# Performance work log

Measured on AMD Instinct MI355X. Metric: run time of the kernel, lower is better.

## Reference

```python
import jax, jax.numpy as jnp
import numpy as np
from math import sqrt

B, L, S = 4, 2048, 2048
D_MODEL, H = 1024, 16
E = D_MODEL // H  # head dim = 64


def setup_inputs() -> dict:
    key = jax.random.key(0)
    ks = jax.random.split(key, 11)
    s = 1.0 / sqrt(D_MODEL)
    return {
        "queries": jax.random.normal(ks[0], (B, L, D_MODEL), jnp.float32),
        "keys": jax.random.normal(ks[1], (B, S, D_MODEL), jnp.float32),
        "values": jax.random.normal(ks[2], (B, S, D_MODEL), jnp.float32),
        "Wq": jax.random.normal(ks[3], (D_MODEL, D_MODEL), jnp.float32) * s,
        "bq": jax.random.normal(ks[4], (D_MODEL,), jnp.float32) * s,
        "Wk": jax.random.normal(ks[5], (D_MODEL, D_MODEL), jnp.float32) * s,
        "bk": jax.random.normal(ks[6], (D_MODEL,), jnp.float32) * s,
        "Wv": jax.random.normal(ks[7], (D_MODEL, D_MODEL), jnp.float32) * s,
        "bv": jax.random.normal(ks[8], (D_MODEL,), jnp.float32) * s,
        "Wo": jax.random.normal(ks[9], (D_MODEL, D_MODEL), jnp.float32) * s,
        "bo": jax.random.normal(ks[10], (D_MODEL,), jnp.float32) * s,
    }


def reference(queries, keys, values, Wq, bq, Wk, bk, Wv, bv, Wo, bo):
    # QKV projections, split heads: [B, L/S, H, E]
    q = (queries @ Wq + bq).reshape(B, L, H, E)
    k = (keys @ Wk + bk).reshape(B, S, H, E)
    v = (values @ Wv + bv).reshape(B, S, H, E)
    scale = 1.0 / sqrt(E)
    scores = jnp.einsum('blhe,bshe->bhls', q, k)  # [B,H,L,S]
    A = jax.nn.softmax(scale * scores, axis=-1)   # dropout is identity in eval
    out = jnp.einsum('bhls,bshd->blhd', A, v).reshape(B, L, H * E)
    return out @ Wo + bo
```

## Files before the change

### kernel.cpp

```cpp
#include <hip/hip_runtime.h>
#include <hip/hip_bf16.h>

typedef unsigned short u16;
typedef unsigned int u32;
using short8 = __attribute__((ext_vector_type(8))) short;
using f32x4  = __attribute__((ext_vector_type(4))) float;
using f32x16 = __attribute__((ext_vector_type(16))) float;
using u32x2  = __attribute__((ext_vector_type(2))) unsigned int;
using u32x4  = __attribute__((ext_vector_type(4))) unsigned int;

#define B_  4
#define L_  2048
#define S_  2048
#define DM  1024
#define H_  16
#define E_  64

__device__ __forceinline__ u16 f2bf(float f) {
  union { float f; unsigned u; } v; v.f = f;
  unsigned u = v.u;
  unsigned r = (u + 0x7fffu + ((u >> 16) & 1u)) >> 16;
  return (u16)r;
}

__device__ __forceinline__ float exp2a(float x) {
  float r; asm("v_exp_f32 %0, %1" : "=v"(r) : "v"(x)); return r;
}

__device__ __forceinline__ u32 cvtpk(float lo, float hi) {
  u32 r; asm("v_cvt_pk_bf16_f32 %0, %1, %2" : "=v"(r) : "v"(lo), "v"(hi));
  return r;
}

__device__ __forceinline__ f32x4 mfma16(short8 a, short8 b, f32x4 c) {
  return __builtin_amdgcn_mfma_f32_16x16x32_bf16(a, b, c, 0, 0, 0);
}

__device__ __forceinline__ f32x16 mfma32(short8 a, short8 b, f32x16 c) {
  return __builtin_amdgcn_mfma_f32_32x32x16_bf16(a, b, c, 0, 0, 0);
}

__device__ __forceinline__ void gload_lds16(const u16* g, u16* l) {
  __builtin_amdgcn_global_load_lds(
      (const __attribute__((address_space(1))) unsigned int*)(const void*)g,
      (__attribute__((address_space(3))) unsigned int*)(void*)l, 16, 0, 0);
}

__global__ __launch_bounds__(256) void transp_all(const float* __restrict__ w0,
                                                  const float* __restrict__ w1,
                                                  const float* __restrict__ w2,
                                                  const float* __restrict__ w3,
                                                  u16* __restrict__ t0,
                                                  u16* __restrict__ t1,
                                                  u16* __restrict__ t2,
                                                  u16* __restrict__ t3) {
  const float* W = blockIdx.z == 0 ? w0 : blockIdx.z == 1 ? w1 :
                   blockIdx.z == 2 ? w2 : w3;
  u16* Wt = blockIdx.z == 0 ? t0 : blockIdx.z == 1 ? t1 :
            blockIdx.z == 2 ? t2 : t3;
  __shared__ float t[32][33];
  int tx = threadIdx.x & 31, ty = (threadIdx.x >> 5) & 7;
#pragma unroll
  for (int j = 0; j < 32; j += 8)
    t[ty + j][tx] = W[(size_t)(blockIdx.y * 32 + ty + j) * DM + blockIdx.x * 32 + tx];
  __syncthreads();
#pragma unroll
  for (int j = 0; j < 32; j += 8)
    Wt[(size_t)(blockIdx.x * 32 + ty + j) * DM + blockIdx.y * 32 + tx] = f2bf(t[tx][ty + j]);
}

template <int EPI>
__device__ __forceinline__ void gemm_body(const float* __restrict__ A,
                                          const u16* __restrict__ Bt,
                                          const float* __restrict__ bias,
                                          void* __restrict__ Cout,
                                          int M, int N, int K, float oscale,
                                          int bx, int by) {
  __shared__ u16 lA[128 * 32];
  __shared__ u16 lB[128 * 32];
  const int tid = threadIdx.x, wid = tid >> 6, lane = tid & 63;
  const int lr = lane & 15, lh = lane >> 4;
  const int m0 = by * 128, n0 = bx * 128;
  const int wr = wid >> 1, wc = wid & 1;

  f32x4 acc[4][4];
#pragma unroll
  for (int m = 0; m < 4; m++)
#pragma unroll
    for (int n = 0; n < 4; n++) acc[m][n] = (f32x4){0.f, 0.f, 0.f, 0.f};

  const int srow = wid * 16 + (lane >> 2);
  const int scol = (lane & 3) * 8;

  const float* a0p = A + (size_t)(m0 + srow) * K + scol;
  const float* a1p = A + (size_t)(m0 + 64 + srow) * K + scol;

  f32x4 r00 = *(const f32x4*)a0p;
  f32x4 r01 = *(const f32x4*)(a0p + 4);
  f32x4 r10 = *(const f32x4*)a1p;
  f32x4 r11 = *(const f32x4*)(a1p + 4);

  for (int k0 = 0; k0 < K; k0 += 32) {
    gload_lds16(Bt + (size_t)(n0 + srow) * K + k0 + scol, lB + (wid * 16) * 32);
    gload_lds16(Bt + (size_t)(n0 + 64 + srow) * K + k0 + scol, lB + (64 + wid * 16) * 32);
    u32x4 w0 = {cvtpk(r00.x, r00.y), cvtpk(r00.z, r00.w),
                cvtpk(r01.x, r01.y), cvtpk(r01.z, r01.w)};
    u32x4 w1 = {cvtpk(r10.x, r10.y), cvtpk(r10.z, r10.w),
                cvtpk(r11.x, r11.y), cvtpk(r11.z, r11.w)};
    *(u32x4*)(lA + (size_t)srow * 32 + scol) = w0;
    *(u32x4*)(lA + (size_t)(64 + srow) * 32 + scol) = w1;
    if (k0 + 32 < K) {
      r00 = *(const f32x4*)(a0p + k0 + 32);
      r01 = *(const f32x4*)(a0p + k0 + 36);
      r10 = *(const f32x4*)(a1p + k0 + 32);
      r11 = *(const f32x4*)(a1p + k0 + 36);
    }
    __syncthreads();
    short8 af[4], bf[4];
#pragma unroll
    for (int m = 0; m < 4; m++)
      af[m] = *(const short8*)(lA + (wr * 64 + m * 16 + lr) * 32 + lh * 8);
#pragma unroll
    for (int n = 0; n < 4; n++)
      bf[n] = *(const short8*)(lB + (wc * 64 + n * 16 + lr) * 32 + lh * 8);
#pragma unroll
    for (int m = 0; m < 4; m++)
#pragma unroll
      for (int n = 0; n < 4; n++) acc[m][n] = mfma16(af[m], bf[n], acc[m][n]);
    __syncthreads();
  }

#pragma unroll
  for (int m = 0; m < 4; m++) {
    int grow0 = m0 + wr * 64 + m * 16 + lh * 4;
#pragma unroll
    for (int n = 0; n < 4; n++) {
      int gcol = n0 + wc * 64 + n * 16 + lr;
      float bi = bias[gcol];
      float v0 = (acc[m][n][0] + bi) * oscale;
      float v1 = (acc[m][n][1] + bi) * oscale;
      float v2 = (acc[m][n][2] + bi) * oscale;
      float v3 = (acc[m][n][3] + bi) * oscale;
      u32 p01 = cvtpk(v0, v1), p23 = cvtpk(v2, v3);
      u16* C = (u16*)Cout;
#pragma unroll
      for (int r = 0; r < 4; r++) {
        u32 pk = r < 2 ? p01 : p23;
        u16 bv = (r & 1) ? (u16)(pk >> 16) : (u16)(pk & 0xffff);
        int grow = grow0 + r;
        if constexpr (EPI == 0) {
          C[(size_t)grow * N + gcol] = bv;
        } else {
          int bb = grow >> 11, sl = grow & 2047;
          C[((size_t)(bb * DM) + gcol) * S_ + sl] = bv;
        }
      }
    }
  }
}

__global__ __launch_bounds__(256) void gemm_qkv(
    const float* __restrict__ q, const float* __restrict__ k, const float* __restrict__ v,
    const u16* __restrict__ WqT, const u16* __restrict__ WkT, const u16* __restrict__ WvT,
    const float* __restrict__ bq, const float* __restrict__ bk, const float* __restrict__ bv,
    u16* __restrict__ Qp, u16* __restrict__ Kp, u16* __restrict__ Vt, float qsc) {
  int lin = blockIdx.x;
  int swz = (lin & 7) * 192 + (lin >> 3);
  const int bx = swz & 7, by = (swz >> 3) & 63, z = swz >> 9;
  if (z == 0)
    gemm_body<0>(q, WqT, bq, Qp, B_ * L_, DM, DM, qsc, bx, by);
  else if (z == 1)
    gemm_body<0>(k, WkT, bk, Kp, B_ * L_, DM, DM, 1.0f, bx, by);
  else
    gemm_body<1>(v, WvT, bv, Vt, B_ * L_, DM, DM, 1.0f, bx, by);
}

__global__ __launch_bounds__(256) void gemm_out(const u16* __restrict__ A,
                                                const u16* __restrict__ Bt,
                                                const float* __restrict__ bias,
                                                float* __restrict__ C) {
  const int N = DM, K = DM;
  int lin = blockIdx.x;
  int swz = (lin & 7) * 64 + (lin >> 3);
  const int bx = swz & 7, by = swz >> 3;

  __shared__ u16 lA[128 * 128];
  __shared__ u16 lB[128 * 128];
  const int tid = threadIdx.x, wid = tid >> 6, lane = tid & 63;
  const int lr = lane & 15, lh = lane >> 4;
  const int m0 = by * 128, n0 = bx * 128;
  const int wr = wid >> 1, wc = wid & 1;

  f32x4 acc[4][4];
#pragma unroll
  for (int m = 0; m < 4; m++)
#pragma unroll
    for (int n = 0; n < 4; n++) acc[m][n] = (f32x4){0.f, 0.f, 0.f, 0.f};

  const int srw = wid * 4 + (lane >> 4);
  const int scx = ((lane & 15) ^ (srw & 15)) * 8;
  const u16* As = A + (size_t)(m0 + srw) * K + scx;
  const u16* Bs = Bt + (size_t)(n0 + srw) * K + scx;
  u16* lAw = lA + (wid * 4) * 128;
  u16* lBw = lB + (wid * 4) * 128;

  for (int k0 = 0; k0 < K; k0 += 128) {
#pragma unroll
    for (int p = 0; p < 8; p++) {
      gload_lds16(As + (size_t)(p * 16) * K + k0, lAw + p * 16 * 128);
      gload_lds16(Bs + (size_t)(p * 16) * K + k0, lBw + p * 16 * 128);
    }
    __syncthreads();
#pragma unroll
    for (int s = 0; s < 4; s++) {
      short8 af[4], bf[4];
#pragma unroll
      for (int m = 0; m < 4; m++)
        af[m] = *(const short8*)(lA + (wr * 64 + m * 16 + lr) * 128 + ((s * 4 + lh) ^ lr) * 8);
#pragma unroll
      for (int n = 0; n < 4; n++)
        bf[n] = *(const short8*)(lB + (wc * 64 + n * 16 + lr) * 128 + ((s * 4 + lh) ^ lr) * 8);
#pragma unroll
      for (int m = 0; m < 4; m++)
#pragma unroll
        for (int n = 0; n < 4; n++) acc[m][n] = mfma16(af[m], bf[n], acc[m][n]);
    }
    __syncthreads();
  }

#pragma unroll
  for (int m = 0; m < 4; m++) {
    int grow0 = m0 + wr * 64 + m * 16 + lh * 4;
#pragma unroll
    for (int n = 0; n < 4; n++) {
      int gcol = n0 + wc * 64 + n * 16 + lr;
      float bi = bias[gcol];
#pragma unroll
      for (int r = 0; r < 4; r++)
        C[(size_t)(grow0 + r) * N + gcol] = acc[m][n][r] + bi;
    }
  }
}

__global__ __launch_bounds__(512) void attn(const u16* __restrict__ Q,
                                            const u16* __restrict__ Kp,
                                            const u16* __restrict__ Vt,
                                            u16* __restrict__ O) {
  __shared__ u16 lK[2][64 * 64];
  __shared__ u16 lV[2][64 * 64];
  const int tid = threadIdx.x, wid = tid >> 6, lane = tid & 63;
  const int l31 = lane & 31, hi = lane >> 5;

  int lin = blockIdx.x;
  int swz = (lin & 7) * 64 + (lin >> 3);
  const int bh = swz >> 3, q0 = (swz & 7) * 256;
  const int b = bh >> 4, h = bh & 15;
  const int qrow = q0 + wid * 32 + l31;

  const u16* Qb = Q + ((size_t)(b * L_ + qrow)) * DM + h * E_ + hi * 8;
  short8 qf[4];
#pragma unroll
  for (int s = 0; s < 4; s++) qf[s] = *(const short8*)(Qb + s * 16);

  f32x16 o[2];
#pragma unroll
  for (int et = 0; et < 2; et++)
#pragma unroll
    for (int r = 0; r < 16; r++) o[et][r] = 0.f;
  float m_r = -3.0e38f, l_r = 0.f;

  const u16* Kb = Kp + ((size_t)(b * S_)) * DM + h * E_;
  const u16* Vb = Vt + ((size_t)(b * DM + h * E_)) * S_;

  const int srow = wid * 8 + (lane >> 3);
  const u16* srcK = Kb + (size_t)srow * DM + ((lane & 7) ^ (srow & 7)) * 8;
  const u16* srcV = Vb + (size_t)srow * S_ + ((lane & 7) ^ (srow & 7)) * 8;

  const int sxk = (l31 & 7) * 8;
  const int hi4 = hi * 4, hi8 = hi * 8;

  auto stage = [&](int buf, int kb) {
    gload_lds16(srcK + (size_t)kb * DM, lK[buf] + wid * 512);
    gload_lds16(srcV + kb, lV[buf] + wid * 512);
  };

  stage(0, 0);
  const int NT = S_ / 64;
  for (int it = 0; it < NT; ++it) {
    const int buf = it & 1;
    __syncthreads();
    if (it + 1 < NT) stage(buf ^ 1, (it + 1) * 64);

    f32x16 sc[2];
    const u16* kbase = lK[buf] + l31 * 64;
    __builtin_amdgcn_s_setprio(1);
#pragma unroll
    for (int kt = 0; kt < 2; kt++) {
      f32x16 a;
#pragma unroll
      for (int r = 0; r < 16; r++) a[r] = 0.f;
#pragma unroll
      for (int s = 0; s < 4; s++) {
        short8 kf = *(const short8*)(kbase + kt * 2048 + ((s * 16 + hi8) ^ sxk));
        a = mfma32(kf, qf[s], a);
      }
      sc[kt] = a;
    }
    __builtin_amdgcn_s_setprio(0);

    f32x16 mA;
#pragma unroll
    for (int r = 0; r < 16; r++) mA[r] = fmaxf(sc[0][r], sc[1][r]);
#pragma unroll
    for (int r = 0; r < 8; r++) mA[r] = fmaxf(mA[r], mA[r + 8]);
#pragma unroll
    for (int r = 0; r < 4; r++) mA[r] = fmaxf(mA[r], mA[r + 4]);
    float tm = fmaxf(fmaxf(mA[0], mA[1]), fmaxf(mA[2], mA[3]));
    tm = fmaxf(tm, __shfl_xor(tm, 32));

    if (__any(tm > m_r + 8.f)) {
      float mn = fmaxf(m_r, tm);
      float al = exp2a(m_r - mn);
      m_r = mn;
      l_r *= al;
#pragma unroll
      for (int et = 0; et < 2; et++)
#pragma unroll
        for (int r = 0; r < 16; r++) o[et][r] *= al;
    }

    u32 wp[2][8];
    float rs = 0.f;
#pragma unroll
    for (int kt = 0; kt < 2; kt++)
#pragma unroll
      for (int i = 0; i < 8; i++) {
        float p0 = exp2a(sc[kt][2 * i] - m_r);
        float p1 = exp2a(sc[kt][2 * i + 1] - m_r);
        rs += p0 + p1;
        wp[kt][i] = cvtpk(p0, p1);
      }
    rs += __shfl_xor(rs, 32);
    l_r += rs;

    __builtin_amdgcn_s_setprio(1);
#pragma unroll
    for (int et = 0; et < 2; et++) {
      const u16* vp = lV[buf] + (et * 32 + l31) * 64;
#pragma unroll
      for (int kt = 0; kt < 2; kt++)
#pragma unroll
        for (int su = 0; su < 2; su++) {
          int koff = kt * 32 + su * 16 + hi4;
          u32x2 lo = *(const u32x2*)(vp + (koff ^ sxk));
          u32x2 hp = *(const u32x2*)(vp + ((koff + 8) ^ sxk));
          u32x4 vv = {lo.x, lo.y, hp.x, hp.y};
          u32x4 pv = {wp[kt][su * 4 + 0], wp[kt][su * 4 + 1],
                      wp[kt][su * 4 + 2], wp[kt][su * 4 + 3]};
          o[et] = mfma32(*(const short8*)&vv, *(const short8*)&pv, o[et]);
        }
    }
    __builtin_amdgcn_s_setprio(0);
  }

  float inv = 1.f / l_r;
  u16* Ob = O + ((size_t)(b * L_ + qrow)) * DM + h * E_;
#pragma unroll
  for (int et = 0; et < 2; et++)
#pragma unroll
    for (int t = 0; t < 4; t++) {
      u32x2 pk;
      pk.x = cvtpk(o[et][4 * t] * inv, o[et][4 * t + 1] * inv);
      pk.y = cvtpk(o[et][4 * t + 2] * inv, o[et][4 * t + 3] * inv);
      *(u32x2*)(Ob + et * 32 + t * 8 + hi4) = pk;
    }
}

extern "C" void kernel_launch(void* const* d_in, const int* in_sizes, int n_in,
                              void* d_out, int out_size, void* d_ws, size_t ws_size,
                              hipStream_t stream) {
  (void)in_sizes; (void)n_in; (void)out_size; (void)ws_size;
  const float* q  = (const float*)d_in[0];
  const float* k  = (const float*)d_in[1];
  const float* v  = (const float*)d_in[2];
  const float* Wq = (const float*)d_in[3];
  const float* bq = (const float*)d_in[4];
  const float* Wk = (const float*)d_in[5];
  const float* bk = (const float*)d_in[6];
  const float* Wv = (const float*)d_in[7];
  const float* bv = (const float*)d_in[8];
  const float* Wo = (const float*)d_in[9];
  const float* bo = (const float*)d_in[10];

  char* w = (char*)d_ws;
  const size_t ACT = (size_t)B_ * L_ * DM * 2;
  const size_t WT  = (size_t)DM * DM * 2;
  u16* WqT = (u16*)w; w += WT;
  u16* WkT = (u16*)w; w += WT;
  u16* WvT = (u16*)w; w += WT;
  u16* WoT = (u16*)w; w += WT;
  u16* Qp  = (u16*)w; w += ACT;
  u16* Kp  = (u16*)w; w += ACT;
  u16* Vt  = (u16*)w; w += ACT;
  u16* At  = (u16*)w; w += ACT;

  transp_all<<<dim3(32, 32, 4), 256, 0, stream>>>(Wq, Wk, Wv, Wo, WqT, WkT, WvT, WoT);

  const float QSC = 0.125f * 1.44269504089f;
  gemm_qkv<<<dim3(1536), 256, 0, stream>>>(
      q, k, v, WqT, WkT, WvT, bq, bk, bv, Qp, Kp, Vt, QSC);

  attn<<<dim3(512), 512, 0, stream>>>(Qp, Kp, Vt, At);

  gemm_out<<<dim3(512), 256, 0, stream>>>(At, WoT, bo, (float*)d_out);
}
```

Measured before the change: 205.8 us.

## Double GEMM K-tile to 64 with XOR-swizzled LDS layout

The projection GEMM body now stages a 64-wide K slice per iteration instead of 32, halving the number of barrier pairs and loop iterations. LDS tiles for A and B use an XOR swizzle on 16-byte chunks, so the wider 128-byte rows avoid bank conflicts on the MFMA fragment reads. The cost is double the LDS footprint and more prefetch registers for A (eight float4 loads per thread), which may lower occupancy.

```diff
diff --git a/kernel.cpp b/kernel.cpp
--- a/kernel.cpp
+++ b/kernel.cpp
@@ -76,8 +76,8 @@
                                           void* __restrict__ Cout,
                                           int M, int N, int K, float oscale,
                                           int bx, int by) {
-  __shared__ u16 lA[128 * 32];
-  __shared__ u16 lB[128 * 32];
+  __shared__ u16 lA[128 * 64];
+  __shared__ u16 lB[128 * 64];
   const int tid = threadIdx.x, wid = tid >> 6, lane = tid & 63;
   const int lr = lane & 15, lh = lane >> 4;
   const int m0 = by * 128, n0 = bx * 128;
@@ -89,44 +89,54 @@
 #pragma unroll
     for (int n = 0; n < 4; n++) acc[m][n] = (f32x4){0.f, 0.f, 0.f, 0.f};
 
-  const int srow = wid * 16 + (lane >> 2);
-  const int scol = (lane & 3) * 8;
-
-  const float* a0p = A + (size_t)(m0 + srow) * K + scol;
-  const float* a1p = A + (size_t)(m0 + 64 + srow) * K + scol;
-
-  f32x4 r00 = *(const f32x4*)a0p;
-  f32x4 r01 = *(const f32x4*)(a0p + 4);
-  f32x4 r10 = *(const f32x4*)a1p;
-  f32x4 r11 = *(const f32x4*)(a1p + 4);
-
-  for (int k0 = 0; k0 < K; k0 += 32) {
-    gload_lds16(Bt + (size_t)(n0 + srow) * K + k0 + scol, lB + (wid * 16) * 32);
-    gload_lds16(Bt + (size_t)(n0 + 64 + srow) * K + k0 + scol, lB + (64 + wid * 16) * 32);
-    u32x4 w0 = {cvtpk(r00.x, r00.y), cvtpk(r00.z, r00.w),
-                cvtpk(r01.x, r01.y), cvtpk(r01.z, r01.w)};
-    u32x4 w1 = {cvtpk(r10.x, r10.y), cvtpk(r10.z, r10.w),
-                cvtpk(r11.x, r11.y), cvtpk(r11.z, r11.w)};
-    *(u32x4*)(lA + (size_t)srow * 32 + scol) = w0;
-    *(u32x4*)(lA + (size_t)(64 + srow) * 32 + scol) = w1;
-    if (k0 + 32 < K) {
-      r00 = *(const f32x4*)(a0p + k0 + 32);
-      r01 = *(const f32x4*)(a0p + k0 + 36);
-      r10 = *(const f32x4*)(a1p + k0 + 32);
-      r11 = *(const f32x4*)(a1p + k0 + 36);
+  const int sbrow = wid * 32 + (lane >> 3);
+  const u16* Bs = Bt + (size_t)(n0 + sbrow) * K + ((lane & 7) ^ (lane >> 3)) * 8;
+  u16* lBw = lB + (wid * 32) * 64;
+
+  const int sar = wid * 32 + (lane >> 1);
+  const int cb4 = (lane & 1) * 4;
+  const int rx = sar & 7;
+  const float* As = A + (size_t)(m0 + sar) * K + cb4 * 8;
+  u16* lArow = lA + (size_t)sar * 64;
+
+  f32x4 ar[8];
+#pragma unroll
+  for (int j = 0; j < 8; j++) ar[j] = *(const f32x4*)(As + j * 4);
+
+  const int sxr = (lr & 7) * 8;
+
+  for (int k0 = 0; k0 < K; k0 += 64) {
+#pragma unroll
+    for (int p = 0; p < 4; p++)
+      gload_lds16(Bs + (size_t)(p * 8) * K + k0, lBw + p * 8 * 64);
+#pragma unroll
+    for (int j = 0; j < 4; j++) {
+      u32x4 wv = {cvtpk(ar[2 * j].x, ar[2 * j].y),
+                  cvtpk(ar[2 * j].z, ar[2 * j].w),
+                  cvtpk(ar[2 * j + 1].x, ar[2 * j + 1].y),
+                  cvtpk(ar[2 * j + 1].z, ar[2 * j + 1].w)};
+      *(u32x4*)(lArow + ((cb4 + j) ^ rx) * 8) = wv;
+    }
+    if (k0 + 64 < K) {
+#pragma unroll
+      for (int j = 0; j < 8; j++)
+        ar[j] = *(const f32x4*)(As + k0 + 64 + j * 4);
     }
     __syncthreads();
-    short8 af[4], bf[4];
-#pragma unroll
-    for (int m = 0; m < 4; m++)
-      af[m] = *(const short8*)(lA + (wr * 64 + m * 16 + lr) * 32 + lh * 8);
-#pragma unroll
-    for (int n = 0; n < 4; n++)
-      bf[n] = *(const short8*)(lB + (wc * 64 + n * 16 + lr) * 32 + lh * 8);
-#pragma unroll
-    for (int m = 0; m < 4; m++)
-#pragma unroll
-      for (int n = 0; n < 4; n++) acc[m][n] = mfma16(af[m], bf[n], acc[m][n]);
+#pragma unroll
+    for (int s = 0; s < 2; s++) {
+      short8 af[4], bf[4];
+#pragma unroll
+      for (int m = 0; m < 4; m++)
+        af[m] = *(const short8*)(lA + (wr * 64 + m * 16 + lr) * 64 + ((s * 32 + lh * 8) ^ sxr));
+#pragma unroll
+      for (int n = 0; n < 4; n++)
+        bf[n] = *(const short8*)(lB + (wc * 64 + n * 16 + lr) * 64 + ((s * 32 + lh * 8) ^ sxr));
+#pragma unroll
+      for (int m = 0; m < 4; m++)
+#pragma unroll
+        for (int n = 0; n < 4; n++) acc[m][n] = mfma16(af[m], bf[n], acc[m][n]);
+    }
     __syncthreads();
   }
 
```

Measured after the change: 255.3 us. 24.1% more time.
